# Performance work log

Hardware: AMD Instinct MI355X
Metric: run time of the kernel (lower is better)

The kernel has to match this reference:

```python
import jax, jax.numpy as jnp
import numpy as np

N = 100000
E = 600000
IN_DIM = 128
HID = 128


def setup_inputs() -> dict:
    key = jax.random.key(0)
    ks = jax.random.split(key, 12)
    def lin(kw, fan_in, fan_out):
        # torch nn.Linear default init: U(-1/sqrt(fan_in), 1/sqrt(fan_in))
        bound = 1.0 / np.sqrt(fan_in)
        kw1, kw2 = jax.random.split(kw)
        w = jax.random.uniform(kw1, (fan_in, fan_out), jnp.float32, -bound, bound)
        b = jax.random.uniform(kw2, (fan_out,), jnp.float32, -bound, bound)
        return w, b
    x = jax.random.normal(ks[0], (N, IN_DIM), jnp.float32)
    edge_index = jax.random.randint(ks[1], (2, E), 0, N, jnp.int64)
    w1a, b1a = lin(ks[2], IN_DIM, HID)
    w1b, b1b = lin(ks[3], HID, HID)
    w2a, b2a = lin(ks[4], HID, HID)
    w2b, b2b = lin(ks[5], HID, HID)
    wo, bo = lin(ks[6], HID, 1)
    return {"x": x, "edge_index": edge_index,
            "w1a": w1a, "b1a": b1a, "w1b": w1b, "b1b": b1b,
            "w2a": w2a, "b2a": b2a, "w2b": w2b, "b2b": b2b,
            "wo": wo, "bo": bo}


def _gin_conv(x, src, dst, wa, ba, wb, bb):
    # sum-aggregate neighbor features: agg[dst] += x[src]; eps = 0 (GIN default)
    agg = jax.ops.segment_sum(x[src], dst, num_segments=N)
    h = x + agg
    h = jax.nn.relu(h @ wa + ba)
    return h @ wb + bb


def reference(x, edge_index, w1a, b1a, w1b, b1b, w2a, b2a, w2b, b2b, wo, bo):
    src, dst = edge_index[0], edge_index[1]
    h = _gin_conv(x, src, dst, w1a, b1a, w1b, b1b)
    h = _gin_conv(h, src, dst, w2a, b2a, w2b, b2b)
    return (h @ wo + bo).squeeze(-1)  # [N]
```

## Files before the change

### kernel.cpp

```cpp
#include <hip/hip_runtime.h>

typedef unsigned short u16;
typedef unsigned int u32;
typedef __bf16 bf16x8 __attribute__((ext_vector_type(8)));
typedef float f32x4 __attribute__((ext_vector_type(4)));

__device__ __forceinline__ u16 f2bf(float f) {
  union { float f; u32 u; } c; c.f = f;
  return (u16)((c.u + 0x7fffu + ((c.u >> 16) & 1u)) >> 16);
}
__device__ __forceinline__ float2 upk2(u32 v) {
  union { u32 u; float f; } a, b; a.u = v << 16; b.u = v & 0xffff0000u;
  return make_float2(a.f, b.f);
}
__device__ __forceinline__ u32 pk2(float x, float y) {
  return (u32)f2bf(x) | ((u32)f2bf(y) << 16);
}

__global__ __launch_bounds__(256) void k_prep(const float4* __restrict__ x4,
                                              uint2* __restrict__ xb,
                                              int n4, int castBlocks,
                                              const int* __restrict__ dst,
                                              int* __restrict__ counts,
                                              int E, int histBlocks,
                                              const float* __restrict__ w0,
                                              const float* __restrict__ w1,
                                              const float* __restrict__ w2,
                                              const float* __restrict__ w3,
                                              u16* __restrict__ wT) {
  int b = blockIdx.x, t = threadIdx.x;
  if (b < castBlocks) {
    int i = b * 256 + t;
    if (i < n4) {
      float4 v = x4[i];
      xb[i] = make_uint2(pk2(v.x, v.y), pk2(v.z, v.w));
    }
  } else if (b < castBlocks + histBlocks) {
    int e = (b - castBlocks) * 256 + t;
    if (e < E) atomicAdd(&counts[dst[e]], 1);
  } else {
    int id = (b - castBlocks - histBlocks) * 256 + t;
    int w = id >> 14, rem = id & 16383;
    int nn = rem >> 7, kk = rem & 127;
    const float* s = (w == 0) ? w0 : (w == 1) ? w1 : (w == 2) ? w2 : w3;
    wT[id] = f2bf(s[kk * 128 + nn]);
  }
}

__global__ __launch_bounds__(256) void k_scan1(const int* __restrict__ counts,
                                               int* __restrict__ excl,
                                               int* __restrict__ partials, int n) {
  __shared__ int sh[256];
  int b = blockIdx.x, t = threadIdx.x;
  int base = b * 1024 + t * 4;
  int v[4];
#pragma unroll
  for (int j = 0; j < 4; ++j) { int i = base + j; v[j] = (i < n) ? counts[i] : 0; }
  int tot = v[0] + v[1] + v[2] + v[3];
  sh[t] = tot; __syncthreads();
  for (int off = 1; off < 256; off <<= 1) {
    int x = (t >= off) ? sh[t - off] : 0;
    __syncthreads();
    sh[t] += x;
    __syncthreads();
  }
  int run = sh[t] - tot;
#pragma unroll
  for (int j = 0; j < 4; ++j) {
    int i = base + j;
    if (i < n) excl[i] = run;
    run += v[j];
  }
  if (t == 255) partials[b] = sh[255];
}

__global__ __launch_bounds__(256) void k_scan23(int* __restrict__ rowstart,
                                                int* __restrict__ cursor,
                                                const int* __restrict__ partials,
                                                int n, int E, int nb) {
  __shared__ int sh[128];
  int t = threadIdx.x;
  int own = 0;
  if (t < 128) { own = (t < nb) ? partials[t] : 0; sh[t] = own; }
  __syncthreads();
  for (int off = 1; off < 128; off <<= 1) {
    int x = (t >= off && t < 128) ? sh[t - off] : 0;
    __syncthreads();
    if (t < 128) sh[t] += x;
    __syncthreads();
  }
  if (t < 128) sh[t] -= own;
  __syncthreads();
  int i = blockIdx.x * 256 + t;
  if (i < n) {
    int v = rowstart[i] + sh[i >> 10];
    rowstart[i] = v;
    cursor[i] = v;
  }
  if (i == 0) rowstart[n] = E;
}

__global__ __launch_bounds__(256) void k_fill(const int* __restrict__ src,
                                              const int* __restrict__ dst,
                                              int* __restrict__ cursor,
                                              int* __restrict__ edge_src, int E) {
  int e = blockIdx.x * 256 + threadIdx.x;
  if (e < E) {
    int d = dst[e];
    int pos = atomicAdd(&cursor[d], 1);
    edge_src[pos] = src[e];
  }
}

__global__ __launch_bounds__(256) void k_agg(const u32* __restrict__ in,
                                             u32* __restrict__ out,
                                             const int* __restrict__ rowstart,
                                             const int* __restrict__ edge_src, int N) {
  int pair = blockIdx.x * 4 + (threadIdx.x >> 6);
  int lane = threadIdx.x & 63;
  int nodeA = __builtin_amdgcn_readfirstlane(pair * 2);
  if (nodeA >= N) return;
  int nodeB = nodeA + 1;
  bool vB = nodeB < N;
  const u32* __restrict__ col = in + lane;
  float2 accA = upk2(col[(size_t)nodeA * 64]);
  float2 accB = vB ? upk2(col[(size_t)nodeB * 64]) : make_float2(0.f, 0.f);
  int a0 = rowstart[nodeA], a1 = rowstart[nodeA + 1];
  int b0 = a1, b1 = vB ? rowstart[nodeB + 1] : a1;
  int ea = a0, eb = b0;
  while (ea < a1 && eb < b1) {
    int ia[8], ib[8]; float wa[8], wb[8]; u32 va[8], vb8[8];
#pragma unroll
    for (int j = 0; j < 8; ++j) {
      int ej = ea + j; int c = (ej < a1) ? ej : (a1 - 1);
      ia[j] = edge_src[c]; wa[j] = (ej < a1) ? 1.f : 0.f;
      int fj = eb + j; int d = (fj < b1) ? fj : (b1 - 1);
      ib[j] = edge_src[d]; wb[j] = (fj < b1) ? 1.f : 0.f;
    }
#pragma unroll
    for (int j = 0; j < 8; ++j) { va[j] = col[(size_t)ia[j] * 64]; vb8[j] = col[(size_t)ib[j] * 64]; }
#pragma unroll
    for (int j = 0; j < 8; ++j) {
      float2 p = upk2(va[j]);
      accA.x = fmaf(wa[j], p.x, accA.x); accA.y = fmaf(wa[j], p.y, accA.y);
      float2 q = upk2(vb8[j]);
      accB.x = fmaf(wb[j], q.x, accB.x); accB.y = fmaf(wb[j], q.y, accB.y);
    }
    ea += 8; eb += 8;
  }
  while (ea < a1) {
    int ia[8]; float wa[8]; u32 va[8];
#pragma unroll
    for (int j = 0; j < 8; ++j) {
      int ej = ea + j; int c = (ej < a1) ? ej : (a1 - 1);
      ia[j] = edge_src[c]; wa[j] = (ej < a1) ? 1.f : 0.f;
    }
#pragma unroll
    for (int j = 0; j < 8; ++j) va[j] = col[(size_t)ia[j] * 64];
#pragma unroll
    for (int j = 0; j < 8; ++j) {
      float2 p = upk2(va[j]);
      accA.x = fmaf(wa[j], p.x, accA.x); accA.y = fmaf(wa[j], p.y, accA.y);
    }
    ea += 8;
  }
  while (eb < b1) {
    int ib[8]; float wb[8]; u32 vb8[8];
#pragma unroll
    for (int j = 0; j < 8; ++j) {
      int fj = eb + j; int d = (fj < b1) ? fj : (b1 - 1);
      ib[j] = edge_src[d]; wb[j] = (fj < b1) ? 1.f : 0.f;
    }
#pragma unroll
    for (int j = 0; j < 8; ++j) vb8[j] = col[(size_t)ib[j] * 64];
#pragma unroll
    for (int j = 0; j < 8; ++j) {
      float2 q = upk2(vb8[j]);
      accB.x = fmaf(wb[j], q.x, accB.x); accB.y = fmaf(wb[j], q.y, accB.y);
    }
    eb += 8;
  }
  out[(size_t)nodeA * 64 + lane] = pk2(accA.x, accA.y);
  if (vB) out[(size_t)nodeB * 64 + lane] = pk2(accB.x, accB.y);
}

template <bool HEAD>
__global__ __launch_bounds__(256) void k_mlp(const u16* __restrict__ in,
                                             const u16* __restrict__ wAT,
                                             const float* __restrict__ bA,
                                             const u16* __restrict__ wBT,
                                             const float* __restrict__ bB,
                                             const float* __restrict__ wo,
                                             const float* __restrict__ bo,
                                             void* __restrict__ outp, int N) {
  __shared__ u16 lA[64 * 128];
  __shared__ u16 lW[128 * 128];
  const int tid = threadIdx.x;
  const int wave = tid >> 6, lane = tid & 63;
  const int base = blockIdx.x * 64;

#pragma unroll
  for (int it = 0; it < 4; ++it) {
    int id = it * 256 + tid;
    int row = id >> 4, c = id & 15;
    uint4 v = make_uint4(0u, 0u, 0u, 0u);
    if (base + row < N) v = *(const uint4*)&in[(base + row) * 128 + c * 8];
    *(uint4*)&lA[row * 128 + ((c ^ (row & 15)) << 3)] = v;
  }
#pragma unroll
  for (int it = 0; it < 8; ++it) {
    int id = it * 256 + tid;
    int row = id >> 4, c = id & 15;
    uint4 v = *(const uint4*)&wAT[row * 128 + c * 8];
    *(uint4*)&lW[row * 128 + ((c ^ (row & 15)) << 3)] = v;
  }
  __syncthreads();

  const int m16 = lane & 15, quad = lane >> 4;
  const int mrow = wave * 16 + m16;

  bf16x8 aF[4];
#pragma unroll
  for (int ks = 0; ks < 4; ++ks)
    aF[ks] = *(const bf16x8*)&lA[mrow * 128 + (((ks * 4 + quad) ^ m16) << 3)];
  f32x4 acc[8];
#pragma unroll
  for (int t = 0; t < 8; ++t) acc[t] = (f32x4){0.f, 0.f, 0.f, 0.f};
#pragma unroll
  for (int t = 0; t < 8; ++t) {
    int nrow = t * 16 + m16;
#pragma unroll
    for (int ks = 0; ks < 4; ++ks) {
      bf16x8 bF = *(const bf16x8*)&lW[nrow * 128 + (((ks * 4 + quad) ^ m16) << 3)];
      acc[t] = __builtin_amdgcn_mfma_f32_16x16x32_bf16(aF[ks], bF, acc[t], 0, 0, 0);
    }
  }
  __syncthreads();

#pragma unroll
  for (int t = 0; t < 8; ++t) {
    int n = t * 16 + m16;
    float bias = bA[n];
#pragma unroll
    for (int r = 0; r < 4; ++r) {
      int rloc = quad * 4 + r;
      int absrow = wave * 16 + rloc;
      float v = acc[t][r] + bias;
      v = v > 0.f ? v : 0.f;
      lA[absrow * 128 + ((((n >> 3) ^ rloc) << 3) | (n & 7))] = f2bf(v);
    }
  }
#pragma unroll
  for (int it = 0; it < 8; ++it) {
    int id = it * 256 + tid;
    int row = id >> 4, c = id & 15;
    uint4 v = *(const uint4*)&wBT[row * 128 + c * 8];
    *(uint4*)&lW[row * 128 + ((c ^ (row & 15)) << 3)] = v;
  }
  __syncthreads();

#pragma unroll
  for (int ks = 0; ks < 4; ++ks)
    aF[ks] = *(const bf16x8*)&lA[mrow * 128 + (((ks * 4 + quad) ^ m16) << 3)];
#pragma unroll
  for (int t = 0; t < 8; ++t) acc[t] = (f32x4){0.f, 0.f, 0.f, 0.f};
#pragma unroll
  for (int t = 0; t < 8; ++t) {
    int nrow = t * 16 + m16;
#pragma unroll
    for (int ks = 0; ks < 4; ++ks) {
      bf16x8 bF = *(const bf16x8*)&lW[nrow * 128 + (((ks * 4 + quad) ^ m16) << 3)];
      acc[t] = __builtin_amdgcn_mfma_f32_16x16x32_bf16(aF[ks], bF, acc[t], 0, 0, 0);
    }
  }
#pragma unroll
  for (int t = 0; t < 8; ++t) {
    int n = t * 16 + m16;
    float bias = bB[n];
#pragma unroll
    for (int r = 0; r < 4; ++r) {
      int rloc = quad * 4 + r;
      int absrow = wave * 16 + rloc;
      float v = acc[t][r] + bias;
      lA[absrow * 128 + ((((n >> 3) ^ rloc) << 3) | (n & 7))] = f2bf(v);
    }
  }
  __syncthreads();

  if (!HEAD) {
    u16* out = (u16*)outp;
#pragma unroll
    for (int it = 0; it < 4; ++it) {
      int id = it * 256 + tid;
      int row = id >> 4, c = id & 15;
      if (base + row < N) {
        uint4 v = *(const uint4*)&lA[row * 128 + ((c ^ (row & 15)) << 3)];
        *(uint4*)&out[(base + row) * 128 + c * 8] = v;
      }
    }
  } else {
    float* out = (float*)outp;
    int row = tid >> 2, qh = tid & 3;
    float s = 0.f;
#pragma unroll
    for (int j = 0; j < 4; ++j) {
      int c = qh * 4 + j;
      uint4 v = *(const uint4*)&lA[row * 128 + ((c ^ (row & 15)) << 3)];
      const float* w = &wo[c * 8];
      float2 p;
      p = upk2(v.x); s += p.x * w[0] + p.y * w[1];
      p = upk2(v.y); s += p.x * w[2] + p.y * w[3];
      p = upk2(v.z); s += p.x * w[4] + p.y * w[5];
      p = upk2(v.w); s += p.x * w[6] + p.y * w[7];
    }
    s += __shfl_xor(s, 1, 64);
    s += __shfl_xor(s, 2, 64);
    if (qh == 0 && base + row < N) {
      out[base + row] = s + bo[0];
    }
  }
}

extern "C" void kernel_launch(void* const* d_in, const int* in_sizes, int n_in,
                              void* d_out, int out_size, void* d_ws, size_t ws_size,
                              hipStream_t stream) {
  const float* x = (const float*)d_in[0];
  const int* ei = (const int*)d_in[1];
  const int E = in_sizes[1] / 2;
  const int N = in_sizes[0] / 128;
  const int* srcI = ei;
  const int* dstI = ei + E;
  const float* w1a = (const float*)d_in[2];
  const float* b1a = (const float*)d_in[3];
  const float* w1b = (const float*)d_in[4];
  const float* b1b = (const float*)d_in[5];
  const float* w2a = (const float*)d_in[6];
  const float* b2a = (const float*)d_in[7];
  const float* w2b = (const float*)d_in[8];
  const float* b2b = (const float*)d_in[9];
  const float* wo = (const float*)d_in[10];
  const float* bo = (const float*)d_in[11];

  char* ws = (char*)d_ws;
  size_t off = 0;
  auto nx = [&](size_t bytes) {
    size_t o = off;
    off += (bytes + 511) & ~(size_t)511;
    return o;
  };
  int* cursor   = (int*)(ws + nx((size_t)N * 4));
  int* rowstart = (int*)(ws + nx((size_t)(N + 1) * 4));
  int* partials = (int*)(ws + nx(4096));
  int* edge_src = (int*)(ws + nx((size_t)E * 4));
  u16* wT       = (u16*)(ws + nx((size_t)4 * 16384 * 2));
  u16* xb       = (u16*)(ws + nx((size_t)N * 128 * 2));
  u16* bufA     = (u16*)(ws + nx((size_t)N * 128 * 2));
  u16* bufB     = (u16*)(ws + nx((size_t)N * 128 * 2));

  const int nb = (N + 1023) >> 10;
  const int n4 = N * 32;
  const int castBlocks = (n4 + 255) / 256;
  const int histBlocks = (E + 255) / 256;
  const int trBlocks = 256;

  hipMemsetAsync(cursor, 0, (size_t)N * 4, stream);
  k_prep<<<castBlocks + histBlocks + trBlocks, 256, 0, stream>>>(
      (const float4*)x, (uint2*)xb, n4, castBlocks,
      dstI, cursor, E, histBlocks,
      w1a, w1b, w2a, w2b, wT);
  k_scan1<<<nb, 256, 0, stream>>>(cursor, rowstart, partials, N);
  k_scan23<<<(N + 255) / 256, 256, 0, stream>>>(rowstart, cursor, partials, N, E, nb);
  k_fill<<<(E + 255) / 256, 256, 0, stream>>>(srcI, dstI, cursor, edge_src, E);

  const int aggBlocks = (N + 7) / 8;
  k_agg<<<aggBlocks, 256, 0, stream>>>((const u32*)xb, (u32*)bufA, rowstart, edge_src, N);
  k_mlp<false><<<(N + 63) / 64, 256, 0, stream>>>(bufA, wT, b1a, wT + 16384, b1b,
                                                  nullptr, nullptr, bufB, N);
  k_agg<<<aggBlocks, 256, 0, stream>>>((const u32*)bufB, (u32*)xb, rowstart, edge_src, N);
  k_mlp<true><<<(N + 63) / 64, 256, 0, stream>>>(xb, wT + 32768, b2a, wT + 49152, b2b,
                                                 wo, bo, d_out, N);
}
```

Measured before the change: 271.0 us.

## Make MLP kernel persistent with resident weights and register-prefetched input tiles

The MLP kernel becomes a persistent grid of 512 blocks that load both weight matrices into shared memory once and then loop over 64-row tiles. The next tile's input is prefetched into registers while the current tile runs its MFMAs, and biases are held in registers. Each wave now works only on its own 16 rows, so the intra-tile block barriers are gone. This removes the per-tile reload of 64 KB of weights and overlaps global loads with compute. In exchange, shared memory use rises to about 80 KB per block, which lowers occupancy.

```diff
diff --git a/kernel.cpp b/kernel.cpp
--- a/kernel.cpp
+++ b/kernel.cpp
@@ -192,131 +192,149 @@
                                              const float* __restrict__ bB,
                                              const float* __restrict__ wo,
                                              const float* __restrict__ bo,
-                                             void* __restrict__ outp, int N) {
+                                             void* __restrict__ outp,
+                                             int N, int ntiles) {
   __shared__ u16 lA[64 * 128];
-  __shared__ u16 lW[128 * 128];
+  __shared__ u16 lW[2 * 128 * 128];
   const int tid = threadIdx.x;
   const int wave = tid >> 6, lane = tid & 63;
-  const int base = blockIdx.x * 64;
-
-#pragma unroll
-  for (int it = 0; it < 4; ++it) {
+  const int m16 = lane & 15, quad = lane >> 4;
+
+#pragma unroll
+  for (int it = 0; it < 16; ++it) {
     int id = it * 256 + tid;
-    int row = id >> 4, c = id & 15;
-    uint4 v = make_uint4(0u, 0u, 0u, 0u);
-    if (base + row < N) v = *(const uint4*)&in[(base + row) * 128 + c * 8];
-    *(uint4*)&lA[row * 128 + ((c ^ (row & 15)) << 3)] = v;
-  }
-#pragma unroll
-  for (int it = 0; it < 8; ++it) {
-    int id = it * 256 + tid;
-    int row = id >> 4, c = id & 15;
-    uint4 v = *(const uint4*)&wAT[row * 128 + c * 8];
-    *(uint4*)&lW[row * 128 + ((c ^ (row & 15)) << 3)] = v;
-  }
+    int m = id >> 11, rem = id & 2047;
+    int row = rem >> 4, c = rem & 15;
+    const u16* s = m ? wBT : wAT;
+    uint4 v = *(const uint4*)&s[row * 128 + c * 8];
+    *(uint4*)&lW[m * 16384 + row * 128 + ((c ^ (row & 15)) << 3)] = v;
+  }
+
+  float bAr[8], bBr[8];
+#pragma unroll
+  for (int t = 0; t < 8; ++t) { bAr[t] = bA[t * 16 + m16]; bBr[t] = bB[t * 16 + m16]; }
+  float boV = HEAD ? bo[0] : 0.f;
+
   __syncthreads();
 
-  const int m16 = lane & 15, quad = lane >> 4;
   const int mrow = wave * 16 + m16;
 
-  bf16x8 aF[4];
-#pragma unroll
-  for (int ks = 0; ks < 4; ++ks)
-    aF[ks] = *(const bf16x8*)&lA[mrow * 128 + (((ks * 4 + quad) ^ m16) << 3)];
-  f32x4 acc[8];
-#pragma unroll
-  for (int t = 0; t < 8; ++t) acc[t] = (f32x4){0.f, 0.f, 0.f, 0.f};
-#pragma unroll
-  for (int t = 0; t < 8; ++t) {
-    int nrow = t * 16 + m16;
-#pragma unroll
-    for (int ks = 0; ks < 4; ++ks) {
-      bf16x8 bF = *(const bf16x8*)&lW[nrow * 128 + (((ks * 4 + quad) ^ m16) << 3)];
-      acc[t] = __builtin_amdgcn_mfma_f32_16x16x32_bf16(aF[ks], bF, acc[t], 0, 0, 0);
-    }
-  }
-  __syncthreads();
-
-#pragma unroll
-  for (int t = 0; t < 8; ++t) {
-    int n = t * 16 + m16;
-    float bias = bA[n];
-#pragma unroll
-    for (int r = 0; r < 4; ++r) {
-      int rloc = quad * 4 + r;
-      int absrow = wave * 16 + rloc;
-      float v = acc[t][r] + bias;
-      v = v > 0.f ? v : 0.f;
-      lA[absrow * 128 + ((((n >> 3) ^ rloc) << 3) | (n & 7))] = f2bf(v);
-    }
-  }
-#pragma unroll
-  for (int it = 0; it < 8; ++it) {
-    int id = it * 256 + tid;
-    int row = id >> 4, c = id & 15;
-    uint4 v = *(const uint4*)&wBT[row * 128 + c * 8];
-    *(uint4*)&lW[row * 128 + ((c ^ (row & 15)) << 3)] = v;
-  }
-  __syncthreads();
-
-#pragma unroll
-  for (int ks = 0; ks < 4; ++ks)
-    aF[ks] = *(const bf16x8*)&lA[mrow * 128 + (((ks * 4 + quad) ^ m16) << 3)];
-#pragma unroll
-  for (int t = 0; t < 8; ++t) acc[t] = (f32x4){0.f, 0.f, 0.f, 0.f};
-#pragma unroll
-  for (int t = 0; t < 8; ++t) {
-    int nrow = t * 16 + m16;
-#pragma unroll
-    for (int ks = 0; ks < 4; ++ks) {
-      bf16x8 bF = *(const bf16x8*)&lW[nrow * 128 + (((ks * 4 + quad) ^ m16) << 3)];
-      acc[t] = __builtin_amdgcn_mfma_f32_16x16x32_bf16(aF[ks], bF, acc[t], 0, 0, 0);
-    }
-  }
-#pragma unroll
-  for (int t = 0; t < 8; ++t) {
-    int n = t * 16 + m16;
-    float bias = bB[n];
-#pragma unroll
-    for (int r = 0; r < 4; ++r) {
-      int rloc = quad * 4 + r;
-      int absrow = wave * 16 + rloc;
-      float v = acc[t][r] + bias;
-      lA[absrow * 128 + ((((n >> 3) ^ rloc) << 3) | (n & 7))] = f2bf(v);
-    }
-  }
-  __syncthreads();
-
-  if (!HEAD) {
-    u16* out = (u16*)outp;
+  uint4 pf[4];
+  auto gload = [&](int tl) {
 #pragma unroll
     for (int it = 0; it < 4; ++it) {
-      int id = it * 256 + tid;
-      int row = id >> 4, c = id & 15;
-      if (base + row < N) {
+      int gr = tl * 64 + wave * 16 + it * 4 + quad;
+      uint4 v = make_uint4(0u, 0u, 0u, 0u);
+      if (gr < N) v = *(const uint4*)&in[(size_t)gr * 128 + m16 * 8];
+      pf[it] = v;
+    }
+  };
+
+  int tile = blockIdx.x;
+  if (tile < ntiles) gload(tile);
+  for (; tile < ntiles; tile += gridDim.x) {
+#pragma unroll
+    for (int it = 0; it < 4; ++it) {
+      int row = wave * 16 + it * 4 + quad;
+      *(uint4*)&lA[row * 128 + ((m16 ^ (row & 15)) << 3)] = pf[it];
+    }
+    bf16x8 aF[4];
+#pragma unroll
+    for (int ks = 0; ks < 4; ++ks)
+      aF[ks] = *(const bf16x8*)&lA[mrow * 128 + (((ks * 4 + quad) ^ m16) << 3)];
+    int nxt = tile + gridDim.x;
+    if (nxt < ntiles) gload(nxt);
+
+    f32x4 acc[8];
+#pragma unroll
+    for (int t = 0; t < 8; ++t) acc[t] = (f32x4){0.f, 0.f, 0.f, 0.f};
+#pragma unroll
+    for (int t = 0; t < 8; ++t) {
+      int nrow = t * 16 + m16;
+#pragma unroll
+      for (int ks = 0; ks < 4; ++ks) {
+        bf16x8 bF = *(const bf16x8*)&lW[nrow * 128 + (((ks * 4 + quad) ^ m16) << 3)];
+        acc[t] = __builtin_amdgcn_mfma_f32_16x16x32_bf16(aF[ks], bF, acc[t], 0, 0, 0);
+      }
+    }
+#pragma unroll
+    for (int t = 0; t < 8; ++t) {
+      int n = t * 16 + m16;
+#pragma unroll
+      for (int r = 0; r < 4; ++r) {
+        int rloc = quad * 4 + r;
+        int absrow = wave * 16 + rloc;
+        float v = acc[t][r] + bAr[t];
+        v = v > 0.f ? v : 0.f;
+        lA[absrow * 128 + ((((n >> 3) ^ rloc) << 3) | (n & 7))] = f2bf(v);
+      }
+    }
+#pragma unroll
+    for (int ks = 0; ks < 4; ++ks)
+      aF[ks] = *(const bf16x8*)&lA[mrow * 128 + (((ks * 4 + quad) ^ m16) << 3)];
+#pragma unroll
+    for (int t = 0; t < 8; ++t) acc[t] = (f32x4){0.f, 0.f, 0.f, 0.f};
+#pragma unroll
+    for (int t = 0; t < 8; ++t) {
+      int nrow = t * 16 + m16;
+#pragma unroll
+      for (int ks = 0; ks < 4; ++ks) {
+        bf16x8 bF = *(const bf16x8*)&lW[16384 + nrow * 128 + (((ks * 4 + quad) ^ m16) << 3)];
+        acc[t] = __builtin_amdgcn_mfma_f32_16x16x32_bf16(aF[ks], bF, acc[t], 0, 0, 0);
+      }
+    }
+    if (!HEAD) {
+#pragma unroll
+      for (int t = 0; t < 8; ++t) {
+        int n = t * 16 + m16;
+#pragma unroll
+        for (int r = 0; r < 4; ++r) {
+          int rloc = quad * 4 + r;
+          int absrow = wave * 16 + rloc;
+          float v = acc[t][r] + bBr[t];
+          lA[absrow * 128 + ((((n >> 3) ^ rloc) << 3) | (n & 7))] = f2bf(v);
+        }
+      }
+      u16* out = (u16*)outp;
+#pragma unroll
+      for (int it = 0; it < 4; ++it) {
+        int row = wave * 16 + it * 4 + quad;
+        int gr = tile * 64 + row;
+        if (gr < N) {
+          uint4 v = *(const uint4*)&lA[row * 128 + ((m16 ^ (row & 15)) << 3)];
+          *(uint4*)&out[(size_t)gr * 128 + m16 * 8] = v;
+        }
+      }
+    } else {
+#pragma unroll
+      for (int t = 0; t < 8; ++t) {
+        int n = t * 16 + m16;
+#pragma unroll
+        for (int r = 0; r < 4; ++r) {
+          int rloc = quad * 4 + r;
+          int absrow = wave * 16 + rloc;
+          float v = acc[t][r] + bBr[t];
+          lA[absrow * 128 + ((((n >> 3) ^ rloc) << 3) | (n & 7))] = f2bf(v);
+        }
+      }
+      float* out = (float*)outp;
+      int row = wave * 16 + (lane >> 2), qh = lane & 3;
+      float s = 0.f;
+#pragma unroll
+      for (int j = 0; j < 4; ++j) {
+        int c = qh * 4 + j;
         uint4 v = *(const uint4*)&lA[row * 128 + ((c ^ (row & 15)) << 3)];
-        *(uint4*)&out[(base + row) * 128 + c * 8] = v;
-      }
-    }
-  } else {
-    float* out = (float*)outp;
-    int row = tid >> 2, qh = tid & 3;
-    float s = 0.f;
-#pragma unroll
-    for (int j = 0; j < 4; ++j) {
-      int c = qh * 4 + j;
-      uint4 v = *(const uint4*)&lA[row * 128 + ((c ^ (row & 15)) << 3)];
-      const float* w = &wo[c * 8];
-      float2 p;
-      p = upk2(v.x); s += p.x * w[0] + p.y * w[1];
-      p = upk2(v.y); s += p.x * w[2] + p.y * w[3];
-      p = upk2(v.z); s += p.x * w[4] + p.y * w[5];
-      p = upk2(v.w); s += p.x * w[6] + p.y * w[7];
-    }
-    s += __shfl_xor(s, 1, 64);
-    s += __shfl_xor(s, 2, 64);
-    if (qh == 0 && base + row < N) {
-      out[base + row] = s + bo[0];
+        const float* w = &wo[c * 8];
+        float2 p;
+        p = upk2(v.x); s += p.x * w[0] + p.y * w[1];
+        p = upk2(v.y); s += p.x * w[2] + p.y * w[3];
+        p = upk2(v.z); s += p.x * w[4] + p.y * w[5];
+        p = upk2(v.w); s += p.x * w[6] + p.y * w[7];
+      }
+      s += __shfl_xor(s, 1, 64);
+      s += __shfl_xor(s, 2, 64);
+      int gr = tile * 64 + row;
+      if (qh == 0 && gr < N) out[gr] = s + boV;
     }
   }
 }
@@ -373,10 +391,13 @@
   k_fill<<<(E + 255) / 256, 256, 0, stream>>>(srcI, dstI, cursor, edge_src, E);
 
   const int aggBlocks = (N + 7) / 8;
+  const int ntiles = (N + 63) / 64;
+  const int mlpGrid = 512;
+
   k_agg<<<aggBlocks, 256, 0, stream>>>((const u32*)xb, (u32*)bufA, rowstart, edge_src, N);
-  k_mlp<false><<<(N + 63) / 64, 256, 0, stream>>>(bufA, wT, b1a, wT + 16384, b1b,
-                                                  nullptr, nullptr, bufB, N);
+  k_mlp<false><<<mlpGrid, 256, 0, stream>>>(bufA, wT, b1a, wT + 16384, b1b,
+                                            nullptr, nullptr, bufB, N, ntiles);
   k_agg<<<aggBlocks, 256, 0, stream>>>((const u32*)bufB, (u32*)xb, rowstart, edge_src, N);
-  k_mlp<true><<<(N + 63) / 64, 256, 0, stream>>>(xb, wT + 32768, b2a, wT + 49152, b2b,
-                                                 wo, bo, d_out, N);
-}
+  k_mlp<true><<<mlpGrid, 256, 0, stream>>>(xb, wT + 32768, b2a, wT + 49152, b2b,
+                                           wo, bo, d_out, N, ntiles);
+}
```

New measurement: 258.5 us. 4.6% less time.
